# Kernel tuning notes

Hardware: AMD Instinct MI355X
Metric: run time of the kernel (lower is better)

## Reference

```python
import jax, jax.numpy as jnp
import numpy as np

B, L, D = 32, 256, 1024
EPS = 1e-5


def _layernorm(x, w, b):
    m = jnp.mean(x, axis=-1, keepdims=True)
    v = jnp.var(x, axis=-1, keepdims=True)
    return (x - m) * jax.lax.rsqrt(v + EPS) * w + b


def _bitlinear(x, w):
    # BitNet b1.58: ternary weights (per-tensor mean-|w| scale),
    # int8 per-token activations; STE so round() passes gradient through.
    ws = jnp.mean(jnp.abs(w)) + EPS
    wq = jnp.clip(jnp.round(w / ws), -1.0, 1.0) * ws
    wq = w + jax.lax.stop_gradient(wq - w)
    xs = 127.0 / jnp.clip(jnp.max(jnp.abs(x), axis=-1, keepdims=True), EPS, None)
    xq = jnp.clip(jnp.round(x * xs), -128.0, 127.0) / xs
    xq = x + jax.lax.stop_gradient(xq - x)
    return jnp.einsum('bld,od->blo', xq, wq)


def setup_inputs() -> dict:
    key = jax.random.key(0)
    kx, kg, k1, k2 = jax.random.split(key, 4)
    i = np.arange(L)
    # deterministic SHA-256-style rotation wiring
    idx_s0 = np.stack([(i + 7) % L, (i + 18) % L, (i + 3) % L], axis=1)
    idx_s1 = np.stack([(i + 17) % L, (i + 19) % L, (i + 10) % L], axis=1)
    idx_v = np.stack([(i + 32 * j) % L for j in range(1, 9)], axis=1)
    return {
        'x': jax.random.normal(kx, (B, L, D), jnp.float32),
        'ln1_w': jnp.ones((D,), jnp.float32),
        'ln1_b': jnp.zeros((D,), jnp.float32),
        'ln2_w': jnp.ones((D,), jnp.float32),
        'ln2_b': jnp.zeros((D,), jnp.float32),
        'Wg': jax.random.normal(kg, (D, 15 * D), jnp.float32) * 0.02,
        'W1': jax.random.normal(k1, (4 * D, D), jnp.float32) * 0.02,
        'W2': jax.random.normal(k2, (D, 4 * D), jnp.float32) * 0.02,
        'idx_s0': jnp.asarray(idx_s0, jnp.int32),
        'idx_s1': jnp.asarray(idx_s1, jnp.int32),
        'idx_v': jnp.asarray(idx_v, jnp.int32),
    }


def reference(x, ln1_w, ln1_b, ln2_w, ln2_b, Wg, W1, W2, idx_s0, idx_s1, idx_v):
    b = x.shape[0]
    xn = _layernorm(x, ln1_w, ln1_b)  # [B,L,D]

    def gather(idx):  # idx: [L,k] -> [B,L,k*D]
        g = jnp.take(xn, idx.reshape(-1), axis=1)  # [B,L*k,D]
        return g.reshape(b, idx.shape[0], -1)

    combined = jnp.concatenate(
        [xn, gather(idx_s0), gather(idx_s1), gather(idx_v)], axis=-1)  # [B,L,15D]
    x = x + _bitlinear(combined, Wg)
    h = _layernorm(x, ln2_w, ln2_b)
    h = _bitlinear(jax.nn.gelu(_bitlinear(h, W1), approximate=False), W2)
    return x + h
```

## Files before the change

kernel.cpp:

```cpp
#include <hip/hip_runtime.h>
#include <hip/hip_bf16.h>
#include <math.h>
#include <stdint.h>

#define EPS 1e-5f

typedef int v4i __attribute__((ext_vector_type(4)));

__device__ __forceinline__ void glds16(const void* g, void* l) {
  __builtin_amdgcn_global_load_lds(
      (const __attribute__((address_space(1))) void*)g,
      (__attribute__((address_space(3))) void*)l, 16, 0, 0);
}

__device__ __forceinline__ signed char q8(float f, float xs) {
  float r = rintf(f * xs);
  r = fminf(fmaxf(r, -128.f), 127.f);
  return (signed char)(int)r;
}

__device__ __forceinline__ float bf2f(unsigned short h) {
  return __builtin_bit_cast(float, (unsigned)h << 16);
}

__global__ __launch_bounds__(256) void absum3_kernel(const float* __restrict__ Wg,
                                                     const float* __restrict__ W1,
                                                     const float* __restrict__ W2,
                                                     float* __restrict__ out) {
  int blk = blockIdx.x;
  const float* w; long n4; float* o; long lb; long nb;
  if (blk < 512)      { w = Wg; n4 = 3932160; o = &out[0]; lb = blk;       nb = 512; }
  else if (blk < 768) { w = W1; n4 = 1048576; o = &out[1]; lb = blk - 512; nb = 256; }
  else                { w = W2; n4 = 1048576; o = &out[2]; lb = blk - 768; nb = 256; }
  const float4* w4 = (const float4*)w;
  float s = 0.f;
  for (long i = lb * 256 + threadIdx.x; i < n4; i += nb * 256) {
    float4 v = w4[i];
    s += fabsf(v.x) + fabsf(v.y) + fabsf(v.z) + fabsf(v.w);
  }
  for (int off = 32; off; off >>= 1) s += __shfl_down(s, off);
  __shared__ float sb[4];
  int lane = threadIdx.x & 63, wid = threadIdx.x >> 6;
  if (lane == 0) sb[wid] = s;
  __syncthreads();
  if (threadIdx.x == 0) atomicAdd(o, sb[0] + sb[1] + sb[2] + sb[3]);
}

__global__ __launch_bounds__(256) void ternarize3_kernel(const float* __restrict__ Wg,
                                                         const float* __restrict__ W1,
                                                         const float* __restrict__ W2,
                                                         signed char* __restrict__ tg,
                                                         signed char* __restrict__ t1,
                                                         signed char* __restrict__ t2,
                                                         const float* __restrict__ sums) {
  int blk = blockIdx.x;
  const float* w; signed char* t; long n4; float ws; long lb; long nb;
  if (blk < 1024) {
    w = Wg; t = tg; n4 = 3932160; ws = sums[0] * (1.f / 15728640.f) + EPS; lb = blk; nb = 1024;
  } else if (blk < 1536) {
    w = W1; t = t1; n4 = 1048576; ws = sums[1] * (1.f / 4194304.f) + EPS; lb = blk - 1024; nb = 512;
  } else {
    w = W2; t = t2; n4 = 1048576; ws = sums[2] * (1.f / 4194304.f) + EPS; lb = blk - 1536; nb = 512;
  }
  const float4* w4 = (const float4*)w;
  char4* t4 = (char4*)t;
  for (long i = lb * 256 + threadIdx.x; i < n4; i += nb * 256) {
    float4 v = w4[i];
    char4 c;
    c.x = (signed char)(int)fminf(fmaxf(rintf(v.x / ws), -1.f), 1.f);
    c.y = (signed char)(int)fminf(fmaxf(rintf(v.y / ws), -1.f), 1.f);
    c.z = (signed char)(int)fminf(fmaxf(rintf(v.z / ws), -1.f), 1.f);
    c.w = (signed char)(int)fminf(fmaxf(rintf(v.w / ws), -1.f), 1.f);
    t4[i] = c;
  }
}

__global__ __launch_bounds__(256) void ln_rowmax_kernel(const float* __restrict__ x,
                                                        const float* __restrict__ w,
                                                        const float* __restrict__ b,
                                                        float* __restrict__ xn,
                                                        float* __restrict__ rowmax) {
  int m = blockIdx.x;
  int tid = threadIdx.x, lane = tid & 63, wid = tid >> 6;
  __shared__ float sb[4];
  float4 v = ((const float4*)(x + (long)m * 1024))[tid];
  float s = v.x + v.y + v.z + v.w;
  for (int off = 32; off; off >>= 1) s += __shfl_down(s, off);
  if (lane == 0) sb[wid] = s;
  __syncthreads();
  float mean = (sb[0] + sb[1] + sb[2] + sb[3]) * (1.f / 1024.f);
  __syncthreads();
  float dx = v.x - mean, dy = v.y - mean, dz = v.z - mean, dw = v.w - mean;
  float ss = dx * dx + dy * dy + dz * dz + dw * dw;
  for (int off = 32; off; off >>= 1) ss += __shfl_down(ss, off);
  if (lane == 0) sb[wid] = ss;
  __syncthreads();
  float rstd = rsqrtf((sb[0] + sb[1] + sb[2] + sb[3]) * (1.f / 1024.f) + EPS);
  __syncthreads();
  float4 wv = ((const float4*)w)[tid];
  float4 bv = ((const float4*)b)[tid];
  float4 o;
  o.x = dx * rstd * wv.x + bv.x;
  o.y = dy * rstd * wv.y + bv.y;
  o.z = dz * rstd * wv.z + bv.z;
  o.w = dw * rstd * wv.w + bv.w;
  ((float4*)(xn + (long)m * 1024))[tid] = o;
  float mx = fmaxf(fmaxf(fabsf(o.x), fabsf(o.y)), fmaxf(fabsf(o.z), fabsf(o.w)));
  for (int off = 32; off; off >>= 1) mx = fmaxf(mx, __shfl_down(mx, off));
  if (lane == 0) sb[wid] = mx;
  __syncthreads();
  if (tid == 0) rowmax[m] = fmaxf(fmaxf(sb[0], sb[1]), fmaxf(sb[2], sb[3]));
}

__global__ __launch_bounds__(256) void quantA_kernel(const float* __restrict__ xn,
                                                     const int* __restrict__ is0,
                                                     const int* __restrict__ is1,
                                                     const int* __restrict__ iv,
                                                     const float* __restrict__ rowmax,
                                                     const float* __restrict__ sums,
                                                     signed char* __restrict__ Aq,
                                                     float* __restrict__ s1) {
  int m = blockIdx.x;
  int b = m >> 8, l = m & 255;
  const float* rm = rowmax + b * 256;
  int src[15];
  src[0] = l;
#pragma unroll
  for (int j = 0; j < 3; ++j) { src[1 + j] = is0[l * 3 + j]; src[4 + j] = is1[l * 3 + j]; }
#pragma unroll
  for (int j = 0; j < 8; ++j) src[7 + j] = iv[l * 8 + j];
  float c = EPS;
#pragma unroll
  for (int sl = 0; sl < 15; ++sl) c = fmaxf(c, rm[src[sl]]);
  float xs = 127.f / c;
  if (threadIdx.x == 0) s1[m] = (sums[0] * (1.f / 15728640.f) + EPS) * c * (1.f / 127.f);
#pragma unroll
  for (int sl = 0; sl < 15; ++sl) {
    float4 v = ((const float4*)(xn + ((long)(b << 8) + src[sl]) * 1024))[threadIdx.x];
    char4 cc;
    cc.x = q8(v.x, xs); cc.y = q8(v.y, xs); cc.z = q8(v.z, xs); cc.w = q8(v.w, xs);
    *(char4*)&Aq[(long)m * 15360 + sl * 1024 + threadIdx.x * 4] = cc;
  }
}

__global__ __launch_bounds__(256) void ln_quant_acc_kernel(const int* __restrict__ accA,
                                                           const int* accB,
                                                           const float* __restrict__ x,
                                                           const float* __restrict__ s1,
                                                           const float* __restrict__ w,
                                                           const float* __restrict__ bb,
                                                           float* xag,
                                                           signed char* __restrict__ q,
                                                           float* __restrict__ srow,
                                                           const float* __restrict__ sum_ptr,
                                                           float inv_n) {
  int m = blockIdx.x;
  int tid = threadIdx.x, lane = tid & 63, wid = tid >> 6;
  __shared__ float sb[4];
  float sm = s1[m];
  int4 a0 = ((const int4*)(accA + (long)m * 1024))[tid];
  int4 a1 = ((const int4*)(accB + (long)m * 1024))[tid];
  float4 xv = ((const float4*)(x + (long)m * 1024))[tid];
  float4 v;
  v.x = xv.x + sm * (float)(a0.x + a1.x);
  v.y = xv.y + sm * (float)(a0.y + a1.y);
  v.z = xv.z + sm * (float)(a0.z + a1.z);
  v.w = xv.w + sm * (float)(a0.w + a1.w);
  ((float4*)(xag + (long)m * 1024))[tid] = v;
  float s = v.x + v.y + v.z + v.w;
  for (int off = 32; off; off >>= 1) s += __shfl_down(s, off);
  if (lane == 0) sb[wid] = s;
  __syncthreads();
  float mean = (sb[0] + sb[1] + sb[2] + sb[3]) * (1.f / 1024.f);
  __syncthreads();
  float dx = v.x - mean, dy = v.y - mean, dz = v.z - mean, dw = v.w - mean;
  float ss = dx * dx + dy * dy + dz * dz + dw * dw;
  for (int off = 32; off; off >>= 1) ss += __shfl_down(ss, off);
  if (lane == 0) sb[wid] = ss;
  __syncthreads();
  float rstd = rsqrtf((sb[0] + sb[1] + sb[2] + sb[3]) * (1.f / 1024.f) + EPS);
  __syncthreads();
  float4 wv = ((const float4*)w)[tid];
  float4 bv = ((const float4*)bb)[tid];
  float nx = dx * rstd * wv.x + bv.x;
  float ny = dy * rstd * wv.y + bv.y;
  float nz = dz * rstd * wv.z + bv.z;
  float nw = dw * rstd * wv.w + bv.w;
  float mx = fmaxf(fmaxf(fabsf(nx), fabsf(ny)), fmaxf(fabsf(nz), fabsf(nw)));
  for (int off = 32; off; off >>= 1) mx = fmaxf(mx, __shfl_down(mx, off));
  if (lane == 0) sb[wid] = mx;
  __syncthreads();
  float rmax = fmaxf(fmaxf(fmaxf(sb[0], sb[1]), fmaxf(sb[2], sb[3])), EPS);
  float xs = 127.f / rmax;
  char4 c;
  c.x = q8(nx, xs); c.y = q8(ny, xs); c.z = q8(nz, xs); c.w = q8(nw, xs);
  *(char4*)&q[(long)m * 1024 + tid * 4] = c;
  if (tid == 0) srow[m] = (sum_ptr[0] * inv_n + EPS) * rmax * (1.f / 127.f);
}

__global__ __launch_bounds__(256) void rowquant4k_kernel(const unsigned short* __restrict__ g,
                                                         signed char* __restrict__ q,
                                                         float* __restrict__ srow,
                                                         const float* __restrict__ sum_ptr,
                                                         float inv_n) {
  int m = blockIdx.x;
  int tid = threadIdx.x, lane = tid & 63, wid = tid >> 6;
  __shared__ float sb[4];
  const uint4* gr = (const uint4*)(g + (long)m * 4096);
  float f[16];
  float mx = 0.f;
#pragma unroll
  for (int i = 0; i < 2; ++i) {
    uint4 u = gr[tid + i * 256];
    unsigned uu[4] = {u.x, u.y, u.z, u.w};
#pragma unroll
    for (int j = 0; j < 4; ++j) {
      float lo = bf2f((unsigned short)(uu[j] & 0xFFFF));
      float hi = bf2f((unsigned short)(uu[j] >> 16));
      f[i * 8 + j * 2] = lo;
      f[i * 8 + j * 2 + 1] = hi;
      mx = fmaxf(mx, fmaxf(fabsf(lo), fabsf(hi)));
    }
  }
  for (int off = 32; off; off >>= 1) mx = fmaxf(mx, __shfl_down(mx, off));
  if (lane == 0) sb[wid] = mx;
  __syncthreads();
  float rmax = fmaxf(fmaxf(fmaxf(sb[0], sb[1]), fmaxf(sb[2], sb[3])), EPS);
  float xs = 127.f / rmax;
#pragma unroll
  for (int i = 0; i < 2; ++i) {
    char4 c0, c1;
    c0.x = q8(f[i * 8 + 0], xs); c0.y = q8(f[i * 8 + 1], xs);
    c0.z = q8(f[i * 8 + 2], xs); c0.w = q8(f[i * 8 + 3], xs);
    c1.x = q8(f[i * 8 + 4], xs); c1.y = q8(f[i * 8 + 5], xs);
    c1.z = q8(f[i * 8 + 6], xs); c1.w = q8(f[i * 8 + 7], xs);
    long base = (long)m * 4096 + (tid + i * 256) * 8;
    *(char4*)&q[base] = c0;
    *(char4*)&q[base + 4] = c1;
  }
  if (tid == 0) srow[m] = (sum_ptr[0] * inv_n + EPS) * rmax * (1.f / 127.f);
}

__global__ __launch_bounds__(256) void reduce3_kernel(const int* __restrict__ accA,
                                                      const int* __restrict__ accB,
                                                      const float* __restrict__ xag,
                                                      const float* __restrict__ s3,
                                                      float* __restrict__ out) {
  int m = blockIdx.x;
  float sm = s3[m];
  int4 a0 = ((const int4*)(accA + (long)m * 1024))[threadIdx.x];
  int4 a1 = ((const int4*)(accB + (long)m * 1024))[threadIdx.x];
  float4 xv = ((const float4*)(xag + (long)m * 1024))[threadIdx.x];
  float4 o;
  o.x = xv.x + sm * (float)(a0.x + a1.x);
  o.y = xv.y + sm * (float)(a0.y + a1.y);
  o.z = xv.z + sm * (float)(a0.z + a1.z);
  o.w = xv.w + sm * (float)(a0.w + a1.w);
  ((float4*)(out + (long)m * 1024))[threadIdx.x] = o;
}


#define LGKM(n) do { asm volatile("s_waitcnt lgkmcnt(" #n ")" ::: "memory"); \
                     __builtin_amdgcn_sched_barrier(0); } while (0)
#define VMC(n)  do { asm volatile("s_waitcnt vmcnt(" #n ")" ::: "memory");   \
                     __builtin_amdgcn_sched_barrier(0); } while (0)
#define SBAR    __builtin_amdgcn_s_barrier()
#define SCHED0  __builtin_amdgcn_sched_barrier(0)

#define MFQ(Af, Bf, QM, QN)                                                    \
  do {                                                                         \
    __builtin_amdgcn_s_setprio(1);                                             \
    _Pragma("unroll") for (int m2 = 0; m2 < 4; ++m2) {                         \
      _Pragma("unroll") for (int n2 = 0; n2 < 2; ++n2) {                       \
        acc[(QM)*4 + m2][(QN)*2 + n2] = __builtin_amdgcn_mfma_i32_16x16x64_i8( \
            Af[m2][0], Bf[n2][0], acc[(QM)*4 + m2][(QN)*2 + n2], 0, 0, 0);     \
        acc[(QM)*4 + m2][(QN)*2 + n2] = __builtin_amdgcn_mfma_i32_16x16x64_i8( \
            Af[m2][1], Bf[n2][1], acc[(QM)*4 + m2][(QN)*2 + n2], 0, 0, 0);     \
      }                                                                        \
    }                                                                          \
    __builtin_amdgcn_s_setprio(0);                                             \
  } while (0)

#define RDA(arr, BO, QMOFS)                                                    \
  _Pragma("unroll") for (int m2 = 0; m2 < 4; ++m2) {                           \
    arr[m2][0] = *(const v4i*)(pA0 + (BO) + (QMOFS) + m2 * 2048);              \
    arr[m2][1] = *(const v4i*)(pA1 + (BO) + (QMOFS) + m2 * 2048);              \
  }
#define RDB(arr, BO, QNOFS)                                                    \
  _Pragma("unroll") for (int n2 = 0; n2 < 2; ++n2) {                           \
    arr[n2][0] = *(const v4i*)(pB0 + (BO) + (QNOFS) + n2 * 2048);              \
    arr[n2][1] = *(const v4i*)(pB1 + (BO) + (QNOFS) + n2 * 2048);              \
  }

__global__ __launch_bounds__(512, 2) void gemm_i8_p(const signed char* __restrict__ A,
                                                    const signed char* __restrict__ Bw,
                                                    __hip_bfloat16* __restrict__ outh,
                                                    int* __restrict__ iacc0,
                                                    int* __restrict__ iacc1,
                                                    const float* __restrict__ scale,
                                                    int N, long K, int nt, int mode,
                                                    int nM, int nN) {
  __shared__ __align__(16) signed char lds[131072];
  const int tid = threadIdx.x;
  const int lane = tid & 63;
  const int wave = tid >> 6;
  const int wm = wave >> 2, wn = wave & 3;
  const int r15 = lane & 15, quad = lane >> 4, sw = lane & 7;

  const int g = (int)blockIdx.x;
  const int mt = g % nM;
  const int rest = g / nM;
  const int ntl = rest % nN;
  const int z = rest / nN;
  const long m0 = (long)mt * 256, n0 = (long)ntl * 256;
  const signed char* Ab = A + m0 * K;
  const signed char* Bb = Bw + n0 * K;
  const long k0base = (long)z * nt * 128;

  unsigned voff[4];
#pragma unroll
  for (int i = 0; i < 4; ++i) {
    int c = wave * 64 + i * 512 + lane;
    int row = c >> 3;
    int blk = (c & 7) ^ (row & 7);
    voff[i] = (unsigned)row * (unsigned)K + (unsigned)(blk << 4);
  }

  const signed char* pA0 = lds + (wm * 128 + r15) * 128 + ((quad ^ sw) << 4);
  const signed char* pA1 = lds + (wm * 128 + r15) * 128 + (((quad + 4) ^ sw) << 4);
  const signed char* pB0 = lds + 65536 + (wn * 64 + r15) * 128 + ((quad ^ sw) << 4);
  const signed char* pB1 = lds + 65536 + (wn * 64 + r15) * 128 + (((quad + 4) ^ sw) << 4);

  v4i a0[4][2], a1[4][2], b0[2][2], b1[2][2];
  v4i acc[8][4] = {};

#define STAGE(BO, KOFF)                                                        \
  _Pragma("unroll") for (int i = 0; i < 4; ++i) {                              \
    int cb = wave * 64 + i * 512;                                              \
    glds16(Ab + (KOFF) + voff[i], (void*)(lds + (BO) + cb * 16));              \
    glds16(Bb + (KOFF) + voff[i], (void*)(lds + 65536 + (BO) + cb * 16));      \
  }

  STAGE(0, k0base);
  STAGE(32768, k0base + 128);
  VMC(8);
  SBAR;
  RDA(a0, 0, 0);
  RDB(b0, 0, 0);
  SCHED0;

  for (int t = 0; t < nt; ++t) {
    const int bo = (t & 1) << 15;
    const int bn = bo ^ 32768;
    RDB(b1, bo, 4096);
    RDA(a1, bo, 8192);
    SCHED0;
    SBAR;
    LGKM(12);
    MFQ(a0, b0, 0, 0);
    SBAR;
    LGKM(8);
    MFQ(a0, b1, 0, 1);
    LGKM(0);
    SBAR;
    if (t + 2 < nt) { STAGE(bo, k0base + (long)(t + 2) * 128); }
    MFQ(a1, b0, 1, 0);
    if (t + 2 < nt) { VMC(8); }
    else           { VMC(0); }
    SBAR;
    if (t + 1 < nt) {
      RDA(a0, bn, 0);
      RDB(b0, bn, 0);
      SCHED0;
    }
    MFQ(a1, b1, 1, 1);
  }

  if (mode == 2) {
    int* iacc = z ? iacc1 : iacc0;
#pragma unroll
    for (int mi = 0; mi < 8; ++mi) {
#pragma unroll
      for (int r = 0; r < 4; ++r) {
        long m = m0 + wm * 128 + mi * 16 + quad * 4 + r;
        int* arow = iacc + m * N;
#pragma unroll
        for (int ni = 0; ni < 4; ++ni)
          arow[n0 + wn * 64 + ni * 16 + r15] = acc[mi][ni][r];
      }
    }
  } else {
#pragma unroll
    for (int mi = 0; mi < 8; ++mi) {
#pragma unroll
      for (int r = 0; r < 4; ++r) {
        long m = m0 + wm * 128 + mi * 16 + quad * 4 + r;
        float sm = scale[m];
        __hip_bfloat16* orow = outh + m * N;
#pragma unroll
        for (int ni = 0; ni < 4; ++ni) {
          float v = sm * (float)acc[mi][ni][r];
          orow[n0 + wn * 64 + ni * 16 + r15] =
              __float2bfloat16(0.5f * v * (1.f + erff(v * 0.70710678118654752f)));
        }
      }
    }
  }
}

extern "C" void kernel_launch(void* const* d_in, const int* in_sizes, int n_in,
                              void* d_out, int out_size, void* d_ws, size_t ws_size,
                              hipStream_t stream) {
  const float* x    = (const float*)d_in[0];
  const float* ln1w = (const float*)d_in[1];
  const float* ln1b = (const float*)d_in[2];
  const float* ln2w = (const float*)d_in[3];
  const float* ln2b = (const float*)d_in[4];
  const float* Wg   = (const float*)d_in[5];
  const float* W1   = (const float*)d_in[6];
  const float* W2   = (const float*)d_in[7];
  const int* is0    = (const int*)d_in[8];
  const int* is1    = (const int*)d_in[9];
  const int* iv     = (const int*)d_in[10];
  float* out = (float*)d_out;

  char* ws = (char*)d_ws;
  float* sums = (float*)ws;
  signed char* t_g = (signed char*)(ws + 256);
  signed char* t_1 = t_g + 15728640;
  signed char* t_2 = t_1 + 4194304;
  float* rowmax1 = (float*)(t_2 + 4194304);
  float* s1  = rowmax1 + 8192;
  float* s2  = s1 + 8192;
  float* s3  = s2 + 8192;
  float* xag = s3 + 8192;
  int* acc1b = (int*)xag;
  signed char* hq = (signed char*)(xag + 8388608);
  float* xn = (float*)(hq + 8388608);
  int* acc1a = (int*)xn;
  signed char* q3 = (signed char*)xn;
  signed char* Aq = (signed char*)(xn + 8388608);
  unsigned short* gg = (unsigned short*)Aq;
  int* acc3a = (int*)Aq;
  int* acc3b = acc3a + 8192l * 1024;

  hipMemsetAsync(sums, 0, 64, stream);
  absum3_kernel<<<1024, 256, 0, stream>>>(Wg, W1, W2, sums);
  ternarize3_kernel<<<2048, 256, 0, stream>>>(Wg, W1, W2, t_g, t_1, t_2, sums);
  ln_rowmax_kernel<<<8192, 256, 0, stream>>>(x, ln1w, ln1b, xn, rowmax1);
  quantA_kernel<<<8192, 256, 0, stream>>>(xn, is0, is1, iv, rowmax1, sums, Aq, s1);
  gemm_i8_p<<<256, 512, 0, stream>>>(Aq, t_g, nullptr, acc1a, acc1b, nullptr,
                                     1024, 15360L, 60, 2, 32, 4);
  ln_quant_acc_kernel<<<8192, 256, 0, stream>>>(acc1a, acc1b, x, s1, ln2w, ln2b, xag, hq, s2,
                                                &sums[1], 1.f / 4194304.f);
  gemm_i8_p<<<512, 512, 0, stream>>>(hq, t_1, (__hip_bfloat16*)gg, nullptr, nullptr,
                                     s2, 4096, 1024L, 8, 1, 32, 16);
  rowquant4k_kernel<<<8192, 256, 0, stream>>>(gg, q3, s3, &sums[2], 1.f / 4194304.f);
  gemm_i8_p<<<256, 512, 0, stream>>>(q3, t_2, nullptr, acc3a, acc3b, nullptr,
                                     1024, 4096L, 16, 2, 32, 4);
  reduce3_kernel<<<8192, 256, 0, stream>>>(acc3a, acc3b, xag, s3, out);
}
```

Baseline: 534.0 us.

## Interleave LDS fragment reads with MFMA quadrants and peel last iteration

Restructures the int8 GEMM main loop so LDS-to-register fragment loads are split into four small issue groups interleaved between the MFMA quadrants, with finer lgkmcnt waits and fewer barriers per iteration. The final k-iteration is peeled out to drop the conditional tail logic. This aims to hide LDS read latency behind matrix-core work and reduce barrier stalls. It relies on hand-tuned waitcnt values, and the global prefetch is now issued later in the iteration with a full vmcnt(0) wait, which could expose more global-load latency.

```diff
diff --git a/kernel.cpp b/kernel.cpp
--- a/kernel.cpp
+++ b/kernel.cpp
@@ -267,6 +267,33 @@
 #define SBAR    __builtin_amdgcn_s_barrier()
 #define SCHED0  __builtin_amdgcn_sched_barrier(0)
 
+#define RD16(P, O) (*(const v4i*)((P) + (O)))
+
+#define ISS_I0(BO) do { \
+  b1[0][0]=RD16(pB0,(BO)+4096);      b1[0][1]=RD16(pB1,(BO)+4096);            \
+  b1[1][0]=RD16(pB0,(BO)+4096+2048); b1[1][1]=RD16(pB1,(BO)+4096+2048);       \
+  SCHED0;                                                                     \
+  a1[0][0]=RD16(pA0,(BO)+8192);      a1[0][1]=RD16(pA1,(BO)+8192);            \
+  SCHED0; } while (0)
+
+#define ISS_I1(BO) do {                                                       \
+  a1[1][0]=RD16(pA0,(BO)+8192+2048); a1[1][1]=RD16(pA1,(BO)+8192+2048);       \
+  a1[2][0]=RD16(pA0,(BO)+8192+4096); a1[2][1]=RD16(pA1,(BO)+8192+4096);       \
+  a1[3][0]=RD16(pA0,(BO)+8192+6144); a1[3][1]=RD16(pA1,(BO)+8192+6144);       \
+  SCHED0; } while (0)
+
+#define ISS_I2(BO) do {                                                       \
+  a0[0][0]=RD16(pA0,(BO));      a0[0][1]=RD16(pA1,(BO));                      \
+  a0[1][0]=RD16(pA0,(BO)+2048); a0[1][1]=RD16(pA1,(BO)+2048);                 \
+  a0[2][0]=RD16(pA0,(BO)+4096); a0[2][1]=RD16(pA1,(BO)+4096);                 \
+  SCHED0; } while (0)
+
+#define ISS_I3(BO) do {                                                       \
+  a0[3][0]=RD16(pA0,(BO)+6144); a0[3][1]=RD16(pA1,(BO)+6144);                 \
+  b0[0][0]=RD16(pB0,(BO));      b0[0][1]=RD16(pB1,(BO));                      \
+  b0[1][0]=RD16(pB0,(BO)+2048); b0[1][1]=RD16(pB1,(BO)+2048);                 \
+  SCHED0; } while (0)
+
 #define MFQ(Af, Bf, QM, QN)                                                    \
   do {                                                                         \
     __builtin_amdgcn_s_setprio(1);                                             \
@@ -280,17 +307,6 @@
     }                                                                          \
     __builtin_amdgcn_s_setprio(0);                                             \
   } while (0)
-
-#define RDA(arr, BO, QMOFS)                                                    \
-  _Pragma("unroll") for (int m2 = 0; m2 < 4; ++m2) {                           \
-    arr[m2][0] = *(const v4i*)(pA0 + (BO) + (QMOFS) + m2 * 2048);              \
-    arr[m2][1] = *(const v4i*)(pA1 + (BO) + (QMOFS) + m2 * 2048);              \
-  }
-#define RDB(arr, BO, QNOFS)                                                    \
-  _Pragma("unroll") for (int n2 = 0; n2 < 2; ++n2) {                           \
-    arr[n2][0] = *(const v4i*)(pB0 + (BO) + (QNOFS) + n2 * 2048);              \
-    arr[n2][1] = *(const v4i*)(pB1 + (BO) + (QNOFS) + n2 * 2048);              \
-  }
 
 __global__ __launch_bounds__(512, 2) void gemm_i8_p(const signed char* __restrict__ A,
                                                     const signed char* __restrict__ Bw,
@@ -345,34 +361,39 @@
   STAGE(32768, k0base + 128);
   VMC(8);
   SBAR;
-  RDA(a0, 0, 0);
-  RDB(b0, 0, 0);
-  SCHED0;
-
-  for (int t = 0; t < nt; ++t) {
+  ISS_I2(0);
+  ISS_I3(0);
+
+  for (int t = 0; t < nt - 1; ++t) {
     const int bo = (t & 1) << 15;
     const int bn = bo ^ 32768;
-    RDB(b1, bo, 4096);
-    RDA(a1, bo, 8192);
-    SCHED0;
+    ISS_I0(bo);
+    LGKM(6);
+    MFQ(a0, b0, 0, 0);
+    ISS_I1(bo);
+    LGKM(8);
+    MFQ(a0, b1, 0, 1);
+    VMC(0);
     SBAR;
-    LGKM(12);
+    ISS_I2(bn);
+    LGKM(6);
+    MFQ(a1, b0, 1, 0);
+    SBAR;
+    if (t + 2 < nt) { STAGE(bo, k0base + (long)(t + 2) * 128); }
+    ISS_I3(bn);
+    MFQ(a1, b1, 1, 1);
+  }
+
+  {
+    const int bo = ((nt - 1) & 1) << 15;
+    ISS_I0(bo);
+    LGKM(6);
     MFQ(a0, b0, 0, 0);
-    SBAR;
+    ISS_I1(bo);
     LGKM(8);
     MFQ(a0, b1, 0, 1);
     LGKM(0);
-    SBAR;
-    if (t + 2 < nt) { STAGE(bo, k0base + (long)(t + 2) * 128); }
     MFQ(a1, b0, 1, 0);
-    if (t + 2 < nt) { VMC(8); }
-    else           { VMC(0); }
-    SBAR;
-    if (t + 1 < nt) {
-      RDA(a0, bn, 0);
-      RDB(b0, bn, 0);
-      SCHED0;
-    }
     MFQ(a1, b1, 1, 1);
   }
 
```

Measured after the change: 542.0 us. Within noise of the previous version (+1.5%).

## Restructure int8 GEMM main loop staging and LDS read schedule

Applied to the files above, without the earlier changes.

Reorders the int8 MFMA GEMM pipeline. One of the four global-to-LDS load pairs for tile t+1 is now issued at the start of iteration t, and the other three are issued for tile t+2 before the final MFMA quadrant. LDS fragment reads are serialized: each quadrant reads its operands and then fully drains lgkmcnt before its MFMAs, instead of prefetching fragments ahead of compute. The change adds barriers and loses the overlap between LDS reads and MFMA work, in exchange for a possibly smoother spread of global loads.

```diff
diff --git a/kernel.cpp b/kernel.cpp
--- a/kernel.cpp
+++ b/kernel.cpp
@@ -267,6 +267,19 @@
 #define SBAR    __builtin_amdgcn_s_barrier()
 #define SCHED0  __builtin_amdgcn_sched_barrier(0)
 
+#define RD16(P, O) (*(const v4i*)((P) + (O)))
+
+#define RDA(arr, BO, QMOFS)                                                    \
+  do { _Pragma("unroll") for (int m2 = 0; m2 < 4; ++m2) {                      \
+    arr[m2][0] = RD16(pA0, (BO) + (QMOFS) + m2 * 2048);                        \
+    arr[m2][1] = RD16(pA1, (BO) + (QMOFS) + m2 * 2048);                        \
+  } SCHED0; } while (0)
+#define RDB(arr, BO, QNOFS)                                                    \
+  do { _Pragma("unroll") for (int n2 = 0; n2 < 2; ++n2) {                      \
+    arr[n2][0] = RD16(pB0, (BO) + (QNOFS) + n2 * 2048);                        \
+    arr[n2][1] = RD16(pB1, (BO) + (QNOFS) + n2 * 2048);                        \
+  } SCHED0; } while (0)
+
 #define MFQ(Af, Bf, QM, QN)                                                    \
   do {                                                                         \
     __builtin_amdgcn_s_setprio(1);                                             \
@@ -280,17 +293,6 @@
     }                                                                          \
     __builtin_amdgcn_s_setprio(0);                                             \
   } while (0)
-
-#define RDA(arr, BO, QMOFS)                                                    \
-  _Pragma("unroll") for (int m2 = 0; m2 < 4; ++m2) {                           \
-    arr[m2][0] = *(const v4i*)(pA0 + (BO) + (QMOFS) + m2 * 2048);              \
-    arr[m2][1] = *(const v4i*)(pA1 + (BO) + (QMOFS) + m2 * 2048);              \
-  }
-#define RDB(arr, BO, QNOFS)                                                    \
-  _Pragma("unroll") for (int n2 = 0; n2 < 2; ++n2) {                           \
-    arr[n2][0] = *(const v4i*)(pB0 + (BO) + (QNOFS) + n2 * 2048);              \
-    arr[n2][1] = *(const v4i*)(pB1 + (BO) + (QNOFS) + n2 * 2048);              \
-  }
 
 __global__ __launch_bounds__(512, 2) void gemm_i8_p(const signed char* __restrict__ A,
                                                     const signed char* __restrict__ Bw,
@@ -334,46 +336,58 @@
   v4i a0[4][2], a1[4][2], b0[2][2], b1[2][2];
   v4i acc[8][4] = {};
 
-#define STAGE(BO, KOFF)                                                        \
-  _Pragma("unroll") for (int i = 0; i < 4; ++i) {                              \
-    int cb = wave * 64 + i * 512;                                              \
+#define STAGE_PAIR(BO, KOFF, i)                                                \
+  do {                                                                         \
+    int cb = wave * 64 + (i) * 512;                                            \
     glds16(Ab + (KOFF) + voff[i], (void*)(lds + (BO) + cb * 16));              \
     glds16(Bb + (KOFF) + voff[i], (void*)(lds + 65536 + (BO) + cb * 16));      \
-  }
-
-  STAGE(0, k0base);
-  STAGE(32768, k0base + 128);
-  VMC(8);
+  } while (0)
+
+  STAGE_PAIR(0, k0base, 0);
+  STAGE_PAIR(0, k0base, 1);
+  STAGE_PAIR(0, k0base, 2);
+  STAGE_PAIR(0, k0base, 3);
+  if (nt > 1) {
+    STAGE_PAIR(32768, k0base + 128, 0);
+    STAGE_PAIR(32768, k0base + 128, 1);
+    STAGE_PAIR(32768, k0base + 128, 2);
+    VMC(6);
+  } else {
+    VMC(0);
+  }
   SBAR;
-  RDA(a0, 0, 0);
-  RDB(b0, 0, 0);
-  SCHED0;
 
   for (int t = 0; t < nt; ++t) {
     const int bo = (t & 1) << 15;
     const int bn = bo ^ 32768;
+    if (t + 1 < nt) { STAGE_PAIR(bn, k0base + (long)(t + 1) * 128, 3); }
+    RDA(a0, bo, 0);
+    RDB(b0, bo, 0);
+    SBAR;
+    LGKM(0);
+    MFQ(a0, b0, 0, 0);
+    SBAR;
     RDB(b1, bo, 4096);
+    SBAR;
+    LGKM(0);
+    MFQ(a0, b1, 0, 1);
+    SBAR;
     RDA(a1, bo, 8192);
-    SCHED0;
-    SBAR;
-    LGKM(12);
-    MFQ(a0, b0, 0, 0);
-    SBAR;
-    LGKM(8);
-    MFQ(a0, b1, 0, 1);
+    SBAR;
     LGKM(0);
-    SBAR;
-    if (t + 2 < nt) { STAGE(bo, k0base + (long)(t + 2) * 128); }
     MFQ(a1, b0, 1, 0);
-    if (t + 2 < nt) { VMC(8); }
+    SBAR;
+    if (t + 2 < nt) {
+      long kN2 = k0base + (long)(t + 2) * 128;
+      STAGE_PAIR(bo, kN2, 0);
+      STAGE_PAIR(bo, kN2, 1);
+      STAGE_PAIR(bo, kN2, 2);
+    }
+    SBAR;
+    MFQ(a1, b1, 1, 1);
+    if (t + 2 < nt) { VMC(6); }
     else           { VMC(0); }
     SBAR;
-    if (t + 1 < nt) {
-      RDA(a0, bn, 0);
-      RDB(b0, bn, 0);
-      SCHED0;
-    }
-    MFQ(a1, b1, 1, 1);
   }
 
   if (mode == 2) {
```

Measured after the change: 527.3 us. No clear change (-1.2%).
